# Kernel tuning notes

Measured on AMD Instinct MI355X. Metric: run time of the kernel, lower is better.

The kernel has to match this reference:

```python
import jax, jax.numpy as jnp
import numpy as np

LN_EPS = 1e-12


def _layernorm(x, g, b):
    mu = jnp.mean(x, axis=-1, keepdims=True)
    var = jnp.mean(jnp.square(x - mu), axis=-1, keepdims=True)
    return (x - mu) * jax.lax.rsqrt(var + LN_EPS) * g + b


def setup_inputs() -> dict:
    key = jax.random.key(0)
    ks = jax.random.split(key, 8)
    A, EP, H, HI, D = 64, 8, 768, 1536, 100
    Etot = A * EP
    return {
        "E": jax.random.normal(ks[0], (A, Etot, H), dtype=jnp.float32),
        "W1": jax.random.normal(ks[1], (H, HI), dtype=jnp.float32) * 0.02,
        "b1": jnp.zeros((HI,), jnp.float32),
        "ln_g": jnp.ones((HI,), jnp.float32),
        "ln_b": jnp.zeros((HI,), jnp.float32),
        "W2": jax.random.normal(ks[2], (HI, D), dtype=jnp.float32) * 0.02,
        "b2": jnp.zeros((D,), jnp.float32),
        "entity_count": 8,  # uniform entities per step (static)
    }


def reference(E, W1, b1, ln_g, ln_b, W2, b2, entity_count):
    A, Etot, H = E.shape
    EP = int(entity_count)
    D = W2.shape[1]

    # VG head: Linear -> exact GELU -> LayerNorm(eps=1e-12) -> Linear
    h = E.reshape(-1, H) @ W1 + b1                       # [A*Etot, 2H]
    h = _layernorm(jax.nn.gelu(h, approximate=False), ln_g, ln_b)
    logits = h @ W2 + b2                                 # [A*Etot, D]
    # reshape(A, Etot, D).permute(1,0,2) -> [Etot, A, D]
    VG_logits = logits.reshape(A, Etot, D).transpose(1, 0, 2)

    # per-entity logits at its own step: idx_2 = step index of each entity
    steps_of = jnp.arange(Etot) // EP                    # [Etot]
    own = VG_logits[jnp.arange(Etot), steps_of]          # [Etot, D]
    VG_scores = jnp.max(jax.nn.softmax(own, axis=-1), axis=-1)  # [Etot]
    VG_scores_index = jnp.argmax(own, axis=-1)           # [Etot] (argmax of softmax == argmax of logits)

    # Faithful to original loop: b stays -1 (`bbox = b+1` never updates b),
    # so every valid score gathers detection VG_scores_index[-1].
    sel = VG_scores_index[-1]
    # entity e=(m,j) -> VG_logits[e, l, sel]; uniform counts => all (j,k) valid
    g = VG_logits[:, :, sel].reshape(A, EP, A)           # [m, j, l]
    scores = jnp.broadcast_to(
        g.transpose(2, 0, 1)[:, :, :, None], (A, A, EP, EP)
    )                                                    # [l, m, j, k]
    scores = scores[None]                                # [1, A, A, EP, EP]

    VG_scores_index_padded = VG_scores_index.reshape(A, EP)
    return scores, VG_scores, VG_scores_index_padded
```

## Files before the change

### kernel.cpp

```cpp
#include <hip/hip_runtime.h>
#include <hip/hip_bf16.h>
#include <math.h>


typedef __bf16 bf16_t;
typedef __bf16  bf16x8  __attribute__((ext_vector_type(8)));
typedef float   floatx4 __attribute__((ext_vector_type(4)));

__device__ __forceinline__ float gelu_exact(float x) {
    return 0.5f * x * (1.0f + erff(x * 0.7071067811865475f));
}
__device__ __forceinline__ float gelu_fast(float x) {
    const float z = x * (1.0f + 0.044715f * x * x);
    return __fdividef(x, 1.0f + __expf(-1.5957691216f * z));
}

__device__ __forceinline__ void gl_lds16(const bf16_t* g, bf16_t* l) {
    __builtin_amdgcn_global_load_lds(
        (const __attribute__((address_space(1))) void*)g,
        (__attribute__((address_space(3))) void*)l, 16, 0, 0);
}

__global__ __launch_bounds__(256) void prep_trio(
        const float* __restrict__ E, const float* __restrict__ W1,
        bf16_t* __restrict__ Ebf, bf16_t* __restrict__ W1t,
        float* __restrict__ hpart) {
    __shared__ alignas(16) char smemc[16640];
    const int bid = blockIdx.x;
    const int tid = threadIdx.x;

    if (bid < 24576) {
        const int t = bid * 256 + tid;
        float4 v = ((const float4*)E)[t];
        union { bf16_t h[4]; uint2 u; } u;
        u.h[0] = (bf16_t)v.x; u.h[1] = (bf16_t)v.y;
        u.h[2] = (bf16_t)v.z; u.h[3] = (bf16_t)v.w;
        *(uint2*)(Ebf + (size_t)t * 4) = u.u;
    } else if (bid < 24864) {
        float* sT = (float*)smemc;
        const int b  = bid - 24576;
        const int bk = b % 12, bn = b / 12;
        const int k0 = bk * 64, n0 = bn * 64;
        #pragma unroll
        for (int i = 0; i < 16; ++i) {
            const int idx = tid + i * 256;
            const int kk = idx >> 6, nn = idx & 63;
            sT[kk * 65 + nn] = W1[(size_t)(k0 + kk) * 1536 + n0 + nn];
        }
        __syncthreads();
        #pragma unroll
        for (int i = 0; i < 16; ++i) {
            const int idx = tid + i * 256;
            const int nn = idx >> 6, kk = idx & 63;
            W1t[(size_t)(n0 + nn) * 768 + k0 + kk] = (bf16_t)sT[kk * 65 + nn];
        }
    } else {
        float* sE = (float*)smemc;
        const int b  = bid - 24864;
        const int a  = b & 63;
        const int rest = b >> 6;
        const int by = rest % 3, kq = rest / 3;

        const float* Ebase = E + (size_t)(520 * a) * 768 + kq * 192;
        for (int idx = tid; idx < 1536; idx += 256) {
            const int row = idx / 192, i = idx - row * 192;
            sE[idx] = Ebase[(size_t)row * 768 + i];
        }
        __syncthreads();

        const int c0 = by * 512 + tid * 2;
        const float* w1p = W1 + (size_t)(kq * 192) * 1536 + c0;
        float ax[8] = {}, ay[8] = {};
        for (int k = 0; k < 192; ++k) {
            const float2 w = *(const float2*)(w1p + (size_t)k * 1536);
            #pragma unroll
            for (int j = 0; j < 8; ++j) {
                const float e = sE[j * 192 + k];
                ax[j] += w.x * e;
                ay[j] += w.y * e;
            }
        }
        #pragma unroll
        for (int j = 0; j < 8; ++j)
            *(float2*)(hpart + (size_t)(kq * 512 + a * 8 + j) * 1536 + c0)
                = make_float2(ax[j], ay[j]);
    }
}

__global__ __launch_bounds__(256) void own_lnlog(
        const float* __restrict__ hpart, const float* __restrict__ b1,
        const float* __restrict__ lng,  const float* __restrict__ lnb,
        const float* __restrict__ W2,   const float* __restrict__ b2,
        float* __restrict__ own) {
    __shared__ float srow[1536];
    __shared__ float red8[8];
    __shared__ float redl[128];
    const int row = blockIdx.x, tid = threadIdx.x;
    const int lane = tid & 63, wv = tid >> 6;

    float x[6];
    #pragma unroll
    for (int i = 0; i < 6; ++i) {
        const int c = tid + i * 256;
        x[i] = gelu_exact(hpart[(size_t)row * 1536 + c]
                        + hpart[(size_t)(512 + row) * 1536 + c]
                        + hpart[(size_t)(1024 + row) * 1536 + c]
                        + hpart[(size_t)(1536 + row) * 1536 + c] + b1[c]);
    }
    float s = 0.f;
    #pragma unroll
    for (int i = 0; i < 6; ++i) s += x[i];
    #pragma unroll
    for (int o = 32; o > 0; o >>= 1) s += __shfl_xor(s, o, 64);
    if (lane == 0) red8[wv] = s;
    __syncthreads();
    const float mu = (red8[0] + red8[1] + red8[2] + red8[3]) * (1.0f / 1536.0f);

    float s2 = 0.f;
    #pragma unroll
    for (int i = 0; i < 6; ++i) { float d = x[i] - mu; s2 += d * d; }
    #pragma unroll
    for (int o = 32; o > 0; o >>= 1) s2 += __shfl_xor(s2, o, 64);
    if (lane == 0) red8[4 + wv] = s2;
    __syncthreads();
    const float rstd = rsqrtf((red8[4] + red8[5] + red8[6] + red8[7]) * (1.0f / 1536.0f) + 1e-12f);

    #pragma unroll
    for (int i = 0; i < 6; ++i) {
        const int c = tid + i * 256;
        srow[c] = (x[i] - mu) * rstd * lng[c] + lnb[c];
    }
    __syncthreads();

    const int d  = tid & 127;
    const int ks = tid >> 7;
    const int dd = d < 100 ? d : 99;
    float acc = ks ? 0.0f : b2[dd];
    const float* hr = srow + ks * 768;
    for (int k = 0; k < 768; ++k)
        acc += hr[k] * W2[(size_t)(ks * 768 + k) * 100 + dd];
    if (ks) redl[d] = acc;
    __syncthreads();
    if (!ks && d < 100) own[(size_t)row * 100 + d] = acc + redl[d];
}

__global__ __launch_bounds__(512) void finalize(
        const float* __restrict__ own, const float* __restrict__ W2,
        const float* __restrict__ b2,  const float* __restrict__ lng,
        const float* __restrict__ lnb, float* __restrict__ out,
        float* __restrict__ u, float* __restrict__ gwbw) {
    __shared__ int ssel;
    __shared__ float rg[8], rb[8];
    const int e = threadIdx.x;
    const int lane = e & 63, wv = e >> 6;
    const float* r = own + (size_t)e * 100;
    float best = r[0]; int bi = 0;
    for (int i = 1; i < 100; ++i) {
        const float v = r[i];
        if (v > best) { best = v; bi = i; }
    }
    float s = 0.f;
    for (int i = 0; i < 100; ++i) s += expf(r[i] - best);
    out[262144 + e] = 1.0f / s;
    out[262656 + e] = (float)bi;
    if (e == 511) ssel = bi;
    __syncthreads();
    const int sel = ssel;

    float gw = 0.f, bw = 0.f;
    #pragma unroll
    for (int c = e; c < 1536; c += 512) {
        const float wv2 = W2[(size_t)c * 100 + sel];
        const float uu = lng[c] * wv2;
        u[c] = uu;
        gw += uu;
        bw += lnb[c] * wv2;
    }
    #pragma unroll
    for (int o = 32; o > 0; o >>= 1) {
        gw += __shfl_xor(gw, o, 64);
        bw += __shfl_xor(bw, o, 64);
    }
    if (lane == 0) { rg[wv] = gw; rb[wv] = bw; }
    __syncthreads();
    if (e == 0) {
        float G = 0.f, B = 0.f;
        #pragma unroll
        for (int i = 0; i < 8; ++i) { G += rg[i]; B += rb[i]; }
        gwbw[0] = G;
        gwbw[1] = B + b2[sel];
    }
}

__global__ __launch_bounds__(256) void gemm1p(
        const bf16_t* __restrict__ A, const bf16_t* __restrict__ Bt,
        const float* __restrict__ bias, const float* __restrict__ u,
        float* __restrict__ pS1, float* __restrict__ pS2,
        float* __restrict__ pD) {
    constexpr int K = 768;
    __shared__ alignas(16) char smem[36864];
    bf16_t* sA = (bf16_t*)smem;
    bf16_t* sB = sA + 128 * 64;

    const int linear = blockIdx.x + gridDim.x * blockIdx.y;
    const int xcd  = linear & 7;
    const int slot = linear >> 3;
    const int bx = slot % gridDim.x;
    const int by = (slot / gridDim.x) * 8 + xcd;

    const int tid  = threadIdx.x;
    const int lane = tid & 63;
    const int wave = tid >> 6;
    const int wr = wave >> 1, wc = wave & 1;
    const int m0 = by * 128;
    const int n0 = bx * 128;
    const int q  = lane >> 4;
    const int l15 = lane & 15;

    const bf16_t* gA[4]; const bf16_t* gB[4];
    bf16_t* lA[4]; bf16_t* lB[4];
    #pragma unroll
    for (int c = 0; c < 4; ++c) {
        const int s    = c * 256 + tid;
        const int row  = s >> 3;
        const int col  = s & 7;
        const int gcol = col ^ (row & 7);
        gA[c] = A  + (size_t)(m0 + row) * K + gcol * 8;
        gB[c] = Bt + (size_t)(n0 + row) * K + gcol * 8;
        lA[c] = sA + (c * 256 + wave * 64) * 8;
        lB[c] = sB + (c * 256 + wave * 64) * 8;
    }
    const bf16_t* rA[4]; const bf16_t* rB[4];
    #pragma unroll
    for (int t4 = 0; t4 < 4; ++t4) {
        rA[t4] = sA + (wr * 64 + t4 * 16 + l15) * 64;
        rB[t4] = sB + (wc * 64 + t4 * 16 + l15) * 64;
    }
    const int c0 = ((q)     ^ (lane & 7)) * 8;
    const int c1 = ((4 + q) ^ (lane & 7)) * 8;

    floatx4 acc[4][4] = {};

    #pragma unroll
    for (int kt = 0; kt < 12; ++kt) {
        const int k0 = kt * 64;
        __syncthreads();
        #pragma unroll
        for (int c = 0; c < 4; ++c) {
            gl_lds16(gA[c] + k0, lA[c]);
            gl_lds16(gB[c] + k0, lB[c]);
        }
        __syncthreads();

        #pragma unroll
        for (int ks = 0; ks < 2; ++ks) {
            const int co = ks ? c1 : c0;
            bf16x8 af[4], bfr[4];
            #pragma unroll
            for (int t4 = 0; t4 < 4; ++t4) {
                af[t4]  = *(const bf16x8*)(rA[t4] + co);
                bfr[t4] = *(const bf16x8*)(rB[t4] + co);
            }
            #pragma unroll
            for (int mt = 0; mt < 4; ++mt)
                #pragma unroll
                for (int nt = 0; nt < 4; ++nt)
                    acc[mt][nt] = __builtin_amdgcn_mfma_f32_16x16x32_bf16(
                        af[mt], bfr[nt], acc[mt][nt], 0, 0, 0);
        }
    }

    __syncthreads();
    bf16_t* sh = (bf16_t*)smem;
    float*  su = (float*)(smem + 33280);
    float*  sp = (float*)(smem + 33792);

    if (tid < 128) su[tid] = u[n0 + tid];
    float bias4[4];
    #pragma unroll
    for (int nt = 0; nt < 4; ++nt) bias4[nt] = bias[n0 + wc * 64 + nt * 16 + l15];

    #pragma unroll
    for (int mt = 0; mt < 4; ++mt)
        #pragma unroll
        for (int nt = 0; nt < 4; ++nt)
            #pragma unroll
            for (int r = 0; r < 4; ++r) {
                const int rowl = wr * 64 + mt * 16 + q * 4 + r;
                const int coll = wc * 64 + nt * 16 + l15;
                sh[rowl * 130 + coll] = (bf16_t)gelu_fast(acc[mt][nt][r] + bias4[nt]);
            }
    __syncthreads();

    {
        const int rowl = tid >> 1, half = tid & 1;
        const bf16_t* hp = sh + rowl * 130 + half * 64;
        const float*  up = su + half * 64;
        float s1 = 0.f, s2 = 0.f, dd = 0.f;
        #pragma unroll
        for (int c = 0; c < 64; ++c) {
            const float v = (float)hp[c];
            s1 += v; s2 += v * v; dd += v * up[c];
        }
        sp[tid * 3 + 0] = s1; sp[tid * 3 + 1] = s2; sp[tid * 3 + 2] = dd;
    }
    __syncthreads();
    if (tid < 128) {
        const float* p0 = sp + (2 * tid) * 3;
        const float* p1 = sp + (2 * tid + 1) * 3;
        const size_t idx = (size_t)bx * 32768 + (m0 + tid);
        pS1[idx] = p0[0] + p1[0];
        pS2[idx] = p0[1] + p1[1];
        pD[idx]  = p0[2] + p1[2];
    }
}

__global__ __launch_bounds__(256) void out_scores(
        const float* __restrict__ pS1, const float* __restrict__ pS2,
        const float* __restrict__ pD,  const float* __restrict__ gwbw,
        float* __restrict__ out) {
    const int t = blockIdx.x * 256 + threadIdx.x;
    float s1 = 0.f, s2 = 0.f, d = 0.f;
    #pragma unroll
    for (int nt = 0; nt < 12; ++nt) {
        const size_t idx = (size_t)nt * 32768 + t;
        s1 += pS1[idx]; s2 += pS2[idx]; d += pD[idx];
    }
    const float mu   = s1 * (1.0f / 1536.0f);
    const float var  = s2 * (1.0f / 1536.0f) - mu * mu;
    const float rstd = rsqrtf(var + 1e-12f);
    const float v = rstd * (d - mu * gwbw[0]) + gwbw[1];
    const float4 f = make_float4(v, v, v, v);
    float4* o = (float4*)(out + (size_t)t * 8);
    o[0] = f; o[1] = f;
}

extern "C" void kernel_launch(void* const* d_in, const int* in_sizes, int n_in,
                              void* d_out, int out_size, void* d_ws, size_t ws_size,
                              hipStream_t stream) {
    const float* E   = (const float*)d_in[0];
    const float* W1  = (const float*)d_in[1];
    const float* b1  = (const float*)d_in[2];
    const float* lng = (const float*)d_in[3];
    const float* lnb = (const float*)d_in[4];
    const float* W2  = (const float*)d_in[5];
    const float* b2  = (const float*)d_in[6];
    float* out = (float*)d_out;

    char* w = (char*)d_ws;
    auto carve = [&](size_t bytes) {
        void* p = (void*)w;
        w += (bytes + 255) & ~(size_t)255;
        return p;
    };
    bf16_t* Ebf   = (bf16_t*)carve((size_t)25165824 * 2);
    bf16_t* W1t   = (bf16_t*)carve((size_t)1536 * 768 * 2);
    float*  hpart = (float*)carve((size_t)4 * 512 * 1536 * 4);
    float*  own   = (float*)carve((size_t)512 * 100 * 4);
    float*  u     = (float*)carve(1536 * 4);
    float*  gwbw  = (float*)carve(256);
    float*  pS1   = (float*)carve((size_t)12 * 32768 * 4);
    float*  pS2   = (float*)carve((size_t)12 * 32768 * 4);
    float*  pD    = (float*)carve((size_t)12 * 32768 * 4);

    prep_trio<<<25632, 256, 0, stream>>>(E, W1, Ebf, W1t, hpart);
    own_lnlog<<<512, 256, 0, stream>>>(hpart, b1, lng, lnb, W2, b2, own);
    finalize<<<1, 512, 0, stream>>>(own, W2, b2, lng, lnb, out, u, gwbw);
    gemm1p<<<dim3(12, 256), 256, 0, stream>>>(Ebf, W1t, b1, u, pS1, pS2, pD);
    out_scores<<<128, 256, 0, stream>>>(pS1, pS2, pD, gwbw, out);
}
```

Measured before the change: 361.7 us.

## Fuse E fp32-to-bf16 conversion into GEMM A-tile loading

Drops the separate pass that converted all of E to bf16 in a workspace buffer, which meant a full read of E plus a write and re-read of the bf16 copy. The GEMM now reads fp32 E directly, converts to bf16 in registers and stores the swizzled tile to LDS, while B keeps using async global-to-LDS loads. This removes a large memory round trip and one workspace buffer. In exchange, the GEMM's A loads become synchronous register loads of twice as many bytes, and each A tile is re-read by the 12 column blocks.

```diff
diff --git a/kernel.cpp b/kernel.cpp
--- a/kernel.cpp
+++ b/kernel.cpp
@@ -21,25 +21,16 @@
         (__attribute__((address_space(3))) void*)l, 16, 0, 0);
 }
 
-__global__ __launch_bounds__(256) void prep_trio(
+__global__ __launch_bounds__(256) void prep_duo(
         const float* __restrict__ E, const float* __restrict__ W1,
-        bf16_t* __restrict__ Ebf, bf16_t* __restrict__ W1t,
-        float* __restrict__ hpart) {
+        bf16_t* __restrict__ W1t, float* __restrict__ hpart) {
     __shared__ alignas(16) char smemc[16640];
     const int bid = blockIdx.x;
     const int tid = threadIdx.x;
 
-    if (bid < 24576) {
-        const int t = bid * 256 + tid;
-        float4 v = ((const float4*)E)[t];
-        union { bf16_t h[4]; uint2 u; } u;
-        u.h[0] = (bf16_t)v.x; u.h[1] = (bf16_t)v.y;
-        u.h[2] = (bf16_t)v.z; u.h[3] = (bf16_t)v.w;
-        *(uint2*)(Ebf + (size_t)t * 4) = u.u;
-    } else if (bid < 24864) {
+    if (bid < 288) {
         float* sT = (float*)smemc;
-        const int b  = bid - 24576;
-        const int bk = b % 12, bn = b / 12;
+        const int bk = bid % 12, bn = bid / 12;
         const int k0 = bk * 64, n0 = bn * 64;
         #pragma unroll
         for (int i = 0; i < 16; ++i) {
@@ -56,7 +47,7 @@
         }
     } else {
         float* sE = (float*)smemc;
-        const int b  = bid - 24864;
+        const int b  = bid - 288;
         const int a  = b & 63;
         const int rest = b >> 6;
         const int by = rest % 3, kq = rest / 3;
@@ -193,7 +184,7 @@
 }
 
 __global__ __launch_bounds__(256) void gemm1p(
-        const bf16_t* __restrict__ A, const bf16_t* __restrict__ Bt,
+        const float* __restrict__ E, const bf16_t* __restrict__ Bt,
         const float* __restrict__ bias, const float* __restrict__ u,
         float* __restrict__ pS1, float* __restrict__ pS2,
         float* __restrict__ pD) {
@@ -217,18 +208,17 @@
     const int q  = lane >> 4;
     const int l15 = lane & 15;
 
-    const bf16_t* gA[4]; const bf16_t* gB[4];
-    bf16_t* lA[4]; bf16_t* lB[4];
+    const float* gAf[4];
+    const bf16_t* gB[4]; bf16_t* lB[4];
     #pragma unroll
     for (int c = 0; c < 4; ++c) {
         const int s    = c * 256 + tid;
         const int row  = s >> 3;
         const int col  = s & 7;
         const int gcol = col ^ (row & 7);
-        gA[c] = A  + (size_t)(m0 + row) * K + gcol * 8;
-        gB[c] = Bt + (size_t)(n0 + row) * K + gcol * 8;
-        lA[c] = sA + (c * 256 + wave * 64) * 8;
-        lB[c] = sB + (c * 256 + wave * 64) * 8;
+        gAf[c] = E  + (size_t)(m0 + row) * K + gcol * 8;
+        gB[c]  = Bt + (size_t)(n0 + row) * K + gcol * 8;
+        lB[c]  = sB + (c * 256 + wave * 64) * 8;
     }
     const bf16_t* rA[4]; const bf16_t* rB[4];
     #pragma unroll
@@ -246,9 +236,17 @@
         const int k0 = kt * 64;
         __syncthreads();
         #pragma unroll
+        for (int c = 0; c < 4; ++c) gl_lds16(gB[c] + k0, lB[c]);
+        #pragma unroll
         for (int c = 0; c < 4; ++c) {
-            gl_lds16(gA[c] + k0, lA[c]);
-            gl_lds16(gB[c] + k0, lB[c]);
+            const float4 v0 = *(const float4*)(gAf[c] + k0);
+            const float4 v1 = *(const float4*)(gAf[c] + k0 + 4);
+            bf16x8 hv;
+            hv[0] = (bf16_t)v0.x; hv[1] = (bf16_t)v0.y;
+            hv[2] = (bf16_t)v0.z; hv[3] = (bf16_t)v0.w;
+            hv[4] = (bf16_t)v1.x; hv[5] = (bf16_t)v1.y;
+            hv[6] = (bf16_t)v1.z; hv[7] = (bf16_t)v1.w;
+            *(bf16x8*)(sA + (c * 256 + tid) * 8) = hv;
         }
         __syncthreads();
 
@@ -353,7 +351,6 @@
         w += (bytes + 255) & ~(size_t)255;
         return p;
     };
-    bf16_t* Ebf   = (bf16_t*)carve((size_t)25165824 * 2);
     bf16_t* W1t   = (bf16_t*)carve((size_t)1536 * 768 * 2);
     float*  hpart = (float*)carve((size_t)4 * 512 * 1536 * 4);
     float*  own   = (float*)carve((size_t)512 * 100 * 4);
@@ -363,9 +360,9 @@
     float*  pS2   = (float*)carve((size_t)12 * 32768 * 4);
     float*  pD    = (float*)carve((size_t)12 * 32768 * 4);
 
-    prep_trio<<<25632, 256, 0, stream>>>(E, W1, Ebf, W1t, hpart);
+    prep_duo<<<1056, 256, 0, stream>>>(E, W1, W1t, hpart);
     own_lnlog<<<512, 256, 0, stream>>>(hpart, b1, lng, lnb, W2, b2, own);
     finalize<<<1, 512, 0, stream>>>(own, W2, b2, lng, lnb, out, u, gwbw);
-    gemm1p<<<dim3(12, 256), 256, 0, stream>>>(Ebf, W1t, b1, u, pS1, pS2, pD);
+    gemm1p<<<dim3(12, 256), 256, 0, stream>>>(E, W1t, b1, u, pS1, pS2, pD);
     out_scores<<<128, 256, 0, stream>>>(pS1, pS2, pD, gwbw, out);
 }
```

New measurement: 356.6 us. Within noise of the previous version (-1.4%).
